# Optimization experiments

Hardware: AMD Instinct MI355X
Metric: run time of the kernel (lower is better)

The kernel has to match this reference:

```python
import jax, jax.numpy as jnp
import numpy as np

N_NODES = 50000
N_EDGES = 800000
UNITS = 128
IN_F = 5


def _sage(x, src, dst, inv_deg, Wl, bl, Wr, n):
    # PyG SAGEConv (mean aggr): out = lin_l(mean_{j in N(i)} x_j) + lin_r(x_i)
    agg = jax.ops.segment_sum(x[src], dst, num_segments=n) * inv_deg  # [n, F]
    return agg @ Wl + bl + x @ Wr


def setup_inputs() -> dict:
    key = jax.random.key(0)
    ks = jax.random.split(key, 16)
    x = jax.random.normal(ks[0], (N_NODES, IN_F), dtype=jnp.float32)
    x = x.at[:, 2].set(0.0)  # do_not_flip flag column: all zeros so no -inf masking
    edge_index = jax.random.randint(ks[1], (2, N_EDGES), 0, N_NODES, dtype=jnp.int64)
    batch = jnp.zeros((N_NODES,), dtype=jnp.int32)

    def lin(k, fi, fo):
        s = 1.0 / np.sqrt(fi)
        return jax.random.uniform(k, (fi, fo), jnp.float32, -s, s)

    inp = {
        "x": x, "edge_index": edge_index, "batch": batch,
        # conv_first: SAGEConv(5, units)
        "Wl1": lin(ks[2], IN_F, UNITS), "bl1": jnp.zeros((UNITS,), jnp.float32), "Wr1": lin(ks[3], IN_F, UNITS),
        # conv_common[0]
        "Wl2": lin(ks[4], UNITS, UNITS), "bl2": jnp.zeros((UNITS,), jnp.float32), "Wr2": lin(ks[5], UNITS, UNITS),
        # conv_actor[0]: SAGEConv(units, 1)
        "Wla": lin(ks[6], UNITS, 1), "bla": jnp.zeros((1,), jnp.float32), "Wra": lin(ks[7], UNITS, 1),
        # conv_critic[0]
        "Wlc": lin(ks[8], UNITS, UNITS), "blc": jnp.zeros((UNITS,), jnp.float32), "Wrc": lin(ks[9], UNITS, UNITS),
        # final_critic Linear(units, 1)
        "Wf": lin(ks[10], UNITS, 1), "bf": jnp.zeros((1,), jnp.float32),
    }
    return inp


def reference(x, edge_index, batch, Wl1, bl1, Wr1, Wl2, bl2, Wr2, Wla, bla, Wra, Wlc, blc, Wrc, Wf, bf):
    n = x.shape[0]
    src, dst = edge_index[0], edge_index[1]
    deg = jax.ops.segment_sum(jnp.ones((src.shape[0],), x.dtype), dst, num_segments=n)
    inv_deg = (1.0 / jnp.maximum(deg, 1.0))[:, None]

    do_not_flip = x[:, 2] != 0.0  # [n]

    h = jnp.tanh(_sage(x, src, dst, inv_deg, Wl1, bl1, Wr1, n))
    h = jnp.tanh(_sage(h, src, dst, inv_deg, Wl2, bl2, Wr2, n))

    x_actor = _sage(h, src, dst, inv_deg, Wla, bla, Wra, n)  # [n, 1]
    x_actor = jnp.where(do_not_flip[:, None], -jnp.inf, x_actor)
    x_actor = jax.nn.log_softmax(x_actor, axis=0)

    x_critic = jax.lax.stop_gradient(h)
    x_critic = _sage(x_critic, src, dst, inv_deg, Wlc, blc, Wrc, n)
    x_critic = x_critic @ Wf + bf  # [n, 1]
    # global_mean_pool over batch (1 graph here)
    num_graphs = 1
    gsum = jax.ops.segment_sum(x_critic, batch, num_segments=num_graphs)
    gcnt = jax.ops.segment_sum(jnp.ones((n,), x.dtype), batch, num_segments=num_graphs)
    x_critic = jnp.tanh(gsum / jnp.maximum(gcnt, 1.0)[:, None])
    return (x_actor, x_critic)
```

## Files before the change

kernel.cpp:

```cpp
#include <hip/hip_runtime.h>
#include <cmath>


#define SCAN_B 256

typedef short short8 __attribute__((ext_vector_type(8)));
typedef float f32x4 __attribute__((ext_vector_type(4)));
typedef float f32x2 __attribute__((ext_vector_type(2)));

__device__ __forceinline__ unsigned short f2b(float f) {
    union { float f; unsigned int u; } v; v.f = f;
    unsigned int r = (v.u + 0x7FFFu + ((v.u >> 16) & 1u)) >> 16;
    return (unsigned short)r;
}
__device__ __forceinline__ float b2f_lo(unsigned int u) {
    union { unsigned int u; float f; } v; v.u = u << 16; return v.f;
}
__device__ __forceinline__ float b2f_hi(unsigned int u) {
    union { unsigned int u; float f; } v; v.u = u & 0xFFFF0000u; return v.f;
}

__global__ void k_count(const int* __restrict__ ei, int* __restrict__ deg, int E) {
    int e = blockIdx.x * 256 + threadIdx.x;
    if (e >= E) return;
    atomicAdd(&deg[ei[E + e]], 1);
}

__global__ void k_blocksum(const int* __restrict__ deg, int* __restrict__ bsum, int n) {
    __shared__ int sd[SCAN_B];
    int i = blockIdx.x * SCAN_B + threadIdx.x;
    sd[threadIdx.x] = (i < n) ? deg[i] : 0;
    __syncthreads();
    for (int s = SCAN_B / 2; s > 0; s >>= 1) {
        if (threadIdx.x < s) sd[threadIdx.x] += sd[threadIdx.x + s];
        __syncthreads();
    }
    if (threadIdx.x == 0) bsum[blockIdx.x] = sd[0];
}

__global__ void k_scan_bsum(int* __restrict__ bsum, int nb) {
    __shared__ int sd[1024];
    int t = threadIdx.x;
    int v = (t < nb) ? bsum[t] : 0;
    sd[t] = v;
    __syncthreads();
    for (int off = 1; off < 1024; off <<= 1) {
        int add = (t >= off) ? sd[t - off] : 0;
        __syncthreads();
        sd[t] += add;
        __syncthreads();
    }
    if (t < nb) bsum[t] = sd[t] - v;
}

__global__ void k_scan_final(const int* __restrict__ deg, const int* __restrict__ bsum,
                             int* __restrict__ row_ptr, int* __restrict__ fill_pos,
                             float* __restrict__ inv_deg, int n) {
    __shared__ int sd[SCAN_B];
    int t = threadIdx.x;
    int i = blockIdx.x * SCAN_B + t;
    int v = (i < n) ? deg[i] : 0;
    sd[t] = v;
    __syncthreads();
    for (int off = 1; off < SCAN_B; off <<= 1) {
        int add = (t >= off) ? sd[t - off] : 0;
        __syncthreads();
        sd[t] += add;
        __syncthreads();
    }
    if (i < n) {
        int excl = bsum[blockIdx.x] + sd[t] - v;
        row_ptr[i] = excl;
        fill_pos[i] = excl;
        inv_deg[i] = 1.0f / fmaxf((float)v, 1.0f);
        if (i == n - 1) row_ptr[n] = excl + v;
    }
}

__global__ void k_fill(const int* __restrict__ ei, int* __restrict__ fill_pos,
                       int* __restrict__ edge_src, int E) {
    int e = blockIdx.x * 256 + threadIdx.x;
    if (e >= E) return;
    int src = ei[e];
    int dst = ei[E + e];
    int pos = atomicAdd(&fill_pos[dst], 1);
    edge_src[pos] = src;
}

__global__ void k_agg0(const float* __restrict__ x, const int* __restrict__ row_ptr,
                       const int* __restrict__ edge_src, const float* __restrict__ inv_deg,
                       float* __restrict__ agg0, int n) {
    int i = blockIdx.x * 256 + threadIdx.x;
    if (i >= n) return;
    float a0 = 0, a1 = 0, a2 = 0, a3 = 0, a4 = 0;
    int s = row_ptr[i], e = row_ptr[i + 1];
    for (int t = s; t < e; ++t) {
        const float* xp = x + (size_t)edge_src[t] * 5;
        a0 += xp[0]; a1 += xp[1]; a2 += xp[2]; a3 += xp[3]; a4 += xp[4];
    }
    float iv = inv_deg[i];
    float* o = agg0 + (size_t)i * 5;
    o[0] = a0 * iv; o[1] = a1 * iv; o[2] = a2 * iv; o[3] = a3 * iv; o[4] = a4 * iv;
}

__global__ void k_h1(const float* __restrict__ x, const float* __restrict__ agg0,
                     const float* __restrict__ Wl1, const float* __restrict__ bl1,
                     const float* __restrict__ Wr1, unsigned short* __restrict__ Acat,
                     unsigned int* __restrict__ H1f8u, int n) {
    __shared__ float sA[8][5], sX[8][5];
    int ty = threadIdx.y, tx = threadIdx.x;
    int node = blockIdx.x * 8 + ty;
    if (node < n && tx < 5) {
        sA[ty][tx] = agg0[(size_t)node * 5 + tx];
        sX[ty][tx] = x[(size_t)node * 5 + tx];
    }
    __syncthreads();
    if (node >= n) return;
    int j0 = tx * 4;
    float4 acc = *(const float4*)(bl1 + j0);
#pragma unroll
    for (int k = 0; k < 5; k++) {
        float4 wl = *(const float4*)(Wl1 + k * 128 + j0);
        float4 wr = *(const float4*)(Wr1 + k * 128 + j0);
        float a = sA[ty][k], xx = sX[ty][k];
        acc.x += a * wl.x + xx * wr.x;
        acc.y += a * wl.y + xx * wr.y;
        acc.z += a * wl.z + xx * wr.z;
        acc.w += a * wl.w + xx * wr.w;
    }
    float t0 = tanhf(acc.x), t1 = tanhf(acc.y), t2 = tanhf(acc.z), t3 = tanhf(acc.w);
    uint2 bw;
    bw.x = (unsigned int)f2b(t0) | ((unsigned int)f2b(t1) << 16);
    bw.y = (unsigned int)f2b(t2) | ((unsigned int)f2b(t3) << 16);
    *(uint2*)(Acat + (size_t)node * 256 + 128 + j0) = bw;
    int p = __builtin_amdgcn_cvt_pk_fp8_f32(t0, t1, 0, false);
    p = __builtin_amdgcn_cvt_pk_fp8_f32(t2, t3, p, true);
    H1f8u[(size_t)node * 32 + tx] = (unsigned int)p;
}

__global__ void k_aggc(const unsigned int* __restrict__ H1f8u, const int* __restrict__ row_ptr,
                       const int* __restrict__ edge_src, const float* __restrict__ inv_deg,
                       unsigned short* __restrict__ Acat, int n, int c) {
    int tid = threadIdx.x;
    int grp = tid >> 4;
    int r = tid & 15;
    int node = blockIdx.x * 16 + grp;
    if (node >= n) return;
    int s = row_ptr[node], e = row_ptr[node + 1];
    const unsigned int* base = H1f8u + c * 16 + r;
    float s0 = 0.f, s1 = 0.f, s2 = 0.f, s3 = 0.f;
    int t = s;
    for (; t + 1 < e; t += 2) {
        unsigned int u0 = base[(size_t)edge_src[t] * 32];
        unsigned int u1 = base[(size_t)edge_src[t + 1] * 32];
        f32x2 lo = __builtin_amdgcn_cvt_pk_f32_fp8(u0, false);
        f32x2 hi = __builtin_amdgcn_cvt_pk_f32_fp8(u0, true);
        s0 += lo[0]; s1 += lo[1]; s2 += hi[0]; s3 += hi[1];
        lo = __builtin_amdgcn_cvt_pk_f32_fp8(u1, false);
        hi = __builtin_amdgcn_cvt_pk_f32_fp8(u1, true);
        s0 += lo[0]; s1 += lo[1]; s2 += hi[0]; s3 += hi[1];
    }
    if (t < e) {
        unsigned int u0 = base[(size_t)edge_src[t] * 32];
        f32x2 lo = __builtin_amdgcn_cvt_pk_f32_fp8(u0, false);
        f32x2 hi = __builtin_amdgcn_cvt_pk_f32_fp8(u0, true);
        s0 += lo[0]; s1 += lo[1]; s2 += hi[0]; s3 += hi[1];
    }
    float iv = inv_deg[node];
    uint2 w;
    w.x = (unsigned int)f2b(s0 * iv) | ((unsigned int)f2b(s1 * iv) << 16);
    w.y = (unsigned int)f2b(s2 * iv) | ((unsigned int)f2b(s3 * iv) << 16);
    *(uint2*)(Acat + (size_t)node * 256 + c * 64 + r * 4) = w;
}

__global__ void k_prepw(const float* __restrict__ Wl2, const float* __restrict__ Wr2,
                        unsigned short* __restrict__ WT) {
    int j = blockIdx.x;
    int k = threadIdx.x;
    float v = (k < 128) ? Wl2[(size_t)k * 128 + j] : Wr2[(size_t)(k - 128) * 128 + j];
    WT[(size_t)j * 256 + k] = f2b(v);
}

__global__ void k_prep(const float* __restrict__ Wlc, const float* __restrict__ blc,
                       const float* __restrict__ Wrc, const float* __restrict__ Wf,
                       const float* __restrict__ bf, float* __restrict__ wcomb) {
    int k = threadIdx.x;
    float sl = 0.f, sr = 0.f;
    for (int j = 0; j < 128; j++) {
        float wf = Wf[j];
        sl += Wlc[(size_t)k * 128 + j] * wf;
        sr += Wrc[(size_t)k * 128 + j] * wf;
    }
    wcomb[k] = sl;
    wcomb[128 + k] = sr;
    __shared__ float sd[128];
    sd[k] = blc[k] * Wf[k];
    __syncthreads();
    for (int s = 64; s > 0; s >>= 1) {
        if (k < s) sd[k] += sd[k + s];
        __syncthreads();
    }
    if (k == 0) wcomb[256] = sd[0] + bf[0];
}

__global__ void k_h2_mfma_dots(const unsigned short* __restrict__ Acat,
                               const unsigned short* __restrict__ WT,
                               const float* __restrict__ bl2,
                               const float* __restrict__ Wla,
                               const float* __restrict__ Wra,
                               const float* __restrict__ wcomb,
                               float2* __restrict__ pp, float2* __restrict__ self, int n) {
    int wave = threadIdx.x >> 6;
    int lane = threadIdx.x & 63;
    int r = lane & 15;
    int g = lane >> 4;
    int rowbase = blockIdx.x * 64 + wave * 16;
    int arow = rowbase + r;
    if (arow > n - 1) arow = n - 1;

    short8 a[8];
    const short* ap = (const short*)(Acat + (size_t)arow * 256 + g * 8);
#pragma unroll
    for (int kk = 0; kk < 8; kk++)
        a[kk] = *(const short8*)(ap + kk * 32);

    float ppa[4] = {0, 0, 0, 0}, ppc[4] = {0, 0, 0, 0};
    float pra[4] = {0, 0, 0, 0}, prc[4] = {0, 0, 0, 0};

#pragma unroll
    for (int nt = 0; nt < 8; nt++) {
        f32x4 acc = {0.f, 0.f, 0.f, 0.f};
        const short* bp = (const short*)(WT + (size_t)(nt * 16 + r) * 256 + g * 8);
#pragma unroll
        for (int kk = 0; kk < 8; kk++) {
            short8 b = *(const short8*)(bp + kk * 32);
            acc = __builtin_amdgcn_mfma_f32_16x16x32_bf16(a[kk], b, acc, 0, 0, 0);
        }
        int col = nt * 16 + r;
        float bj  = bl2[col];
        float wa  = Wla[col];
        float wra = Wra[col];
        float wcl = wcomb[col];
        float wcr = wcomb[128 + col];
#pragma unroll
        for (int q = 0; q < 4; q++) {
            float t = tanhf(acc[q] + bj);
            ppa[q] += t * wa;
            ppc[q] += t * wcl;
            pra[q] += t * wra;
            prc[q] += t * wcr;
        }
    }
#pragma unroll
    for (int q = 0; q < 4; q++) {
#pragma unroll
        for (int off = 8; off >= 1; off >>= 1) {
            ppa[q] += __shfl_xor(ppa[q], off);
            ppc[q] += __shfl_xor(ppc[q], off);
            pra[q] += __shfl_xor(pra[q], off);
            prc[q] += __shfl_xor(prc[q], off);
        }
    }
    if (r == 0) {
#pragma unroll
        for (int q = 0; q < 4; q++) {
            int rr = rowbase + g * 4 + q;
            if (rr < n) {
                pp[rr]   = make_float2(ppa[q], ppc[q]);
                self[rr] = make_float2(pra[q], prc[q]);
            }
        }
    }
}

__global__ void k_sagg(const float2* __restrict__ pp, const float2* __restrict__ self,
                       const int* __restrict__ row_ptr, const int* __restrict__ edge_src,
                       const float* __restrict__ inv_deg, const float* __restrict__ x,
                       const float* __restrict__ bla, const float* __restrict__ wcomb,
                       float* __restrict__ actor_s, float* __restrict__ critic_v, int n) {
    int i = blockIdx.x * 256 + threadIdx.x;
    if (i >= n) return;
    int s = row_ptr[i], e = row_ptr[i + 1];
    float sa = 0.f, sc = 0.f;
    for (int t = s; t < e; ++t) {
        float2 v = pp[edge_src[t]];
        sa += v.x; sc += v.y;
    }
    float iv = inv_deg[i];
    float2 sf = self[i];
    float a = sa * iv + sf.x + bla[0];
    if (x[(size_t)i * 5 + 2] != 0.0f) a = -INFINITY;
    actor_s[i] = a;
    critic_v[i] = sc * iv + sf.y + wcomb[256];
}

__global__ void k_reduce(const float* __restrict__ actor_s, const float* __restrict__ critic_v,
                         float* __restrict__ scalars, float* __restrict__ d_out, int n) {
    __shared__ float sm[1024], ss[1024], sc[1024];
    int t = threadIdx.x;
    float m = -INFINITY, sum = 0.f, cs = 0.f;
    for (int i = t; i < n; i += 1024) {
        cs += critic_v[i];
        float s = actor_s[i];
        if (s == -INFINITY) continue;
        if (s > m) {
            sum = sum * expf(m - s);
            m = s;
        }
        sum += expf(s - m);
    }
    sm[t] = m; ss[t] = sum; sc[t] = cs;
    __syncthreads();
    for (int s2 = 512; s2 > 0; s2 >>= 1) {
        if (t < s2) {
            float m2 = sm[t + s2], v2 = ss[t + s2];
            float M = fmaxf(sm[t], m2);
            if (M == -INFINITY) {
                ss[t] = 0.f;
            } else {
                ss[t] = ss[t] * expf(sm[t] - M) + v2 * expf(m2 - M);
            }
            sm[t] = M;
            sc[t] += sc[t + s2];
        }
        __syncthreads();
    }
    if (t == 0) {
        scalars[0] = sm[0] + logf(ss[0]);
        d_out[n] = tanhf(sc[0] / (float)n);
    }
}

__global__ void k_final(const float* __restrict__ actor_s, const float* __restrict__ scalars,
                        float* __restrict__ d_out, int n) {
    int i = blockIdx.x * 256 + threadIdx.x;
    if (i >= n) return;
    d_out[i] = actor_s[i] - scalars[0];
}

extern "C" void kernel_launch(void* const* d_in, const int* in_sizes, int n_in,
                              void* d_out, int out_size, void* d_ws, size_t ws_size,
                              hipStream_t stream) {
    const float* x   = (const float*)d_in[0];
    const int*   ei  = (const int*)d_in[1];
    const float* Wl1 = (const float*)d_in[3];
    const float* bl1 = (const float*)d_in[4];
    const float* Wr1 = (const float*)d_in[5];
    const float* Wl2 = (const float*)d_in[6];
    const float* bl2 = (const float*)d_in[7];
    const float* Wr2 = (const float*)d_in[8];
    const float* Wla = (const float*)d_in[9];
    const float* bla = (const float*)d_in[10];
    const float* Wra = (const float*)d_in[11];
    const float* Wlc = (const float*)d_in[12];
    const float* blc = (const float*)d_in[13];
    const float* Wrc = (const float*)d_in[14];
    const float* Wf  = (const float*)d_in[15];
    const float* bf  = (const float*)d_in[16];

    const int n = in_sizes[0] / 5;
    const int E = in_sizes[1] / 2;
    float* out = (float*)d_out;

    char* w = (char*)d_ws;
    auto alloc = [&](size_t bytes) -> void* {
        void* p = (void*)w;
        w += (bytes + 255) & ~(size_t)255;
        return p;
    };
    int* deg      = (int*)alloc((size_t)n * 4);
    int* row_ptr  = (int*)alloc((size_t)(n + 1) * 4);
    int* fill_pos = (int*)alloc((size_t)n * 4);
    int* bsum     = (int*)alloc(1024 * 4);
    int* edge_src = (int*)alloc((size_t)E * 4);
    float* inv_deg = (float*)alloc((size_t)n * 4);
    float* agg0    = (float*)alloc((size_t)n * 5 * 4);
    unsigned short* Acat = (unsigned short*)alloc((size_t)n * 256 * 2);
    unsigned int* H1f8u  = (unsigned int*)alloc((size_t)n * 128);
    unsigned short* WT   = (unsigned short*)alloc((size_t)128 * 256 * 2);
    float2* pp     = (float2*)alloc((size_t)n * 8);
    float2* selfb  = (float2*)alloc((size_t)n * 8);
    float* actor_s = (float*)alloc((size_t)n * 4);
    float* critic_v= (float*)alloc((size_t)n * 4);
    float* wcomb   = (float*)alloc(260 * 4);
    float* scalars = (float*)alloc(16);

    hipMemsetAsync(deg, 0, (size_t)n * 4, stream);

    const int nbE = (E + 255) / 256;
    const int nbN = (n + 255) / 256;
    const int nbScan = (n + SCAN_B - 1) / SCAN_B;

    k_count<<<nbE, 256, 0, stream>>>(ei, deg, E);
    k_blocksum<<<nbScan, SCAN_B, 0, stream>>>(deg, bsum, n);
    k_scan_bsum<<<1, 1024, 0, stream>>>(bsum, nbScan);
    k_scan_final<<<nbScan, SCAN_B, 0, stream>>>(deg, bsum, row_ptr, fill_pos, inv_deg, n);
    k_fill<<<nbE, 256, 0, stream>>>(ei, fill_pos, edge_src, E);

    k_agg0<<<nbN, 256, 0, stream>>>(x, row_ptr, edge_src, inv_deg, agg0, n);
    k_h1<<<(n + 7) / 8, dim3(32, 8), 0, stream>>>(x, agg0, Wl1, bl1, Wr1, Acat, H1f8u, n);

    k_aggc<<<(n + 15) / 16, 256, 0, stream>>>(H1f8u, row_ptr, edge_src, inv_deg, Acat, n, 0);
    k_aggc<<<(n + 15) / 16, 256, 0, stream>>>(H1f8u, row_ptr, edge_src, inv_deg, Acat, n, 1);

    k_prepw<<<128, 256, 0, stream>>>(Wl2, Wr2, WT);
    k_prep<<<1, 128, 0, stream>>>(Wlc, blc, Wrc, Wf, bf, wcomb);
    k_h2_mfma_dots<<<(n + 63) / 64, 256, 0, stream>>>(Acat, WT, bl2, Wla, Wra, wcomb,
                                                      pp, selfb, n);

    k_sagg<<<nbN, 256, 0, stream>>>(pp, selfb, row_ptr, edge_src, inv_deg, x,
                                    bla, wcomb, actor_s, critic_v, n);
    k_reduce<<<1, 1024, 0, stream>>>(actor_s, critic_v, scalars, out, n);
    k_final<<<nbN, 256, 0, stream>>>(actor_s, scalars, out, n);
}
```

Baseline: 254.7 us.

## Build CSR via two-level bucketed binning instead of global atomic counting sort

Replaces the global-atomic degree count, three-kernel scan and atomic scatter fill with a two-level bucket sort. Edges are first binned into 128-node buckets using shared-memory histograms and per-block atomic reservations, then each bucket is sorted locally in LDS to produce row_ptr, inv_deg and edge_src. This reduces global atomic contention and the scattered writes, and drops the memset. In exchange it makes an extra pass over the edges through an intermediate packed array. The packing assumes source indices fit in 25 bits and at most 512 buckets.

Result: faster. 212.7 us (-16.5%).

```diff
diff --git a/kernel.cpp b/kernel.cpp
--- a/kernel.cpp
+++ b/kernel.cpp
@@ -2,7 +2,11 @@
 #include <cmath>
 
 
-#define SCAN_B 256
+#define NPB_SHIFT 7
+#define NPB 128
+#define MAXNB 512
+#define HBLK 192
+#define CHUNK 8192
 
 typedef short short8 __attribute__((ext_vector_type(8)));
 typedef float f32x4 __attribute__((ext_vector_type(4)));
@@ -13,79 +17,113 @@
     unsigned int r = (v.u + 0x7FFFu + ((v.u >> 16) & 1u)) >> 16;
     return (unsigned short)r;
 }
-__device__ __forceinline__ float b2f_lo(unsigned int u) {
-    union { unsigned int u; float f; } v; v.u = u << 16; return v.f;
-}
-__device__ __forceinline__ float b2f_hi(unsigned int u) {
-    union { unsigned int u; float f; } v; v.u = u & 0xFFFF0000u; return v.f;
-}
-
-__global__ void k_count(const int* __restrict__ ei, int* __restrict__ deg, int E) {
-    int e = blockIdx.x * 256 + threadIdx.x;
-    if (e >= E) return;
-    atomicAdd(&deg[ei[E + e]], 1);
-}
-
-__global__ void k_blocksum(const int* __restrict__ deg, int* __restrict__ bsum, int n) {
-    __shared__ int sd[SCAN_B];
-    int i = blockIdx.x * SCAN_B + threadIdx.x;
-    sd[threadIdx.x] = (i < n) ? deg[i] : 0;
-    __syncthreads();
-    for (int s = SCAN_B / 2; s > 0; s >>= 1) {
-        if (threadIdx.x < s) sd[threadIdx.x] += sd[threadIdx.x + s];
-        __syncthreads();
-    }
-    if (threadIdx.x == 0) bsum[blockIdx.x] = sd[0];
-}
-
-__global__ void k_scan_bsum(int* __restrict__ bsum, int nb) {
-    __shared__ int sd[1024];
+
+
+__global__ void kb_hist(const int* __restrict__ ei, int* __restrict__ partial, int E, int NB) {
+    __shared__ int h[MAXNB];
+    for (int i = threadIdx.x; i < NB; i += 256) h[i] = 0;
+    __syncthreads();
+    for (int i = blockIdx.x * 256 + threadIdx.x; i < E; i += 256 * gridDim.x)
+        atomicAdd(&h[ei[E + i] >> NPB_SHIFT], 1);
+    __syncthreads();
+    for (int b = threadIdx.x; b < NB; b += 256)
+        partial[(size_t)b * HBLK + blockIdx.x] = h[b];
+}
+
+__global__ void kb_scan(const int* __restrict__ partial, int* __restrict__ bucket_base,
+                        int* __restrict__ bucket_cur, int NB) {
+    __shared__ int sd[MAXNB];
     int t = threadIdx.x;
-    int v = (t < nb) ? bsum[t] : 0;
-    sd[t] = v;
-    __syncthreads();
-    for (int off = 1; off < 1024; off <<= 1) {
+    int c = 0;
+    if (t < NB) {
+        const int* p = partial + (size_t)t * HBLK;
+        for (int k = 0; k < HBLK; k++) c += p[k];
+    }
+    sd[t] = c;
+    __syncthreads();
+    for (int off = 1; off < MAXNB; off <<= 1) {
         int add = (t >= off) ? sd[t - off] : 0;
         __syncthreads();
         sd[t] += add;
         __syncthreads();
     }
-    if (t < nb) bsum[t] = sd[t] - v;
-}
-
-__global__ void k_scan_final(const int* __restrict__ deg, const int* __restrict__ bsum,
-                             int* __restrict__ row_ptr, int* __restrict__ fill_pos,
-                             float* __restrict__ inv_deg, int n) {
-    __shared__ int sd[SCAN_B];
+    if (t < NB) {
+        int excl = sd[t] - c;
+        bucket_base[t] = excl;
+        bucket_cur[t] = excl;
+        if (t == NB - 1) bucket_base[NB] = sd[t];
+    }
+}
+
+__global__ void kb_bin(const int* __restrict__ ei, int* __restrict__ bucket_cur,
+                       unsigned int* __restrict__ binned, int E, int NB) {
+    __shared__ int lcnt[MAXNB];
+    __shared__ int lbase[MAXNB];
+    __shared__ int lcur[MAXNB];
+    int s = blockIdx.x * CHUNK;
+    int e = min(E, s + CHUNK);
+    for (int i = threadIdx.x; i < NB; i += 256) lcnt[i] = 0;
+    __syncthreads();
+    for (int i = s + threadIdx.x; i < e; i += 256)
+        atomicAdd(&lcnt[ei[E + i] >> NPB_SHIFT], 1);
+    __syncthreads();
+    for (int b = threadIdx.x; b < NB; b += 256) {
+        int c = lcnt[b];
+        lbase[b] = c ? atomicAdd(&bucket_cur[b], c) : 0;
+        lcur[b] = 0;
+    }
+    __syncthreads();
+    for (int i = s + threadIdx.x; i < e; i += 256) {
+        int src = ei[i];
+        int dst = ei[E + i];
+        int b = dst >> NPB_SHIFT;
+        int pos = lbase[b] + atomicAdd(&lcur[b], 1);
+        binned[pos] = (unsigned int)src | ((unsigned int)(dst & (NPB - 1)) << 25);
+    }
+}
+
+__global__ void kb_csr(const unsigned int* __restrict__ binned, const int* __restrict__ bucket_base,
+                       int* __restrict__ row_ptr, float* __restrict__ inv_deg,
+                       int* __restrict__ edge_src, int n, int NB) {
+    __shared__ int lcnt[NPB];
+    __shared__ int lexcl[NPB];
+    __shared__ int lcur[NPB];
+    int b = blockIdx.x;
     int t = threadIdx.x;
-    int i = blockIdx.x * SCAN_B + t;
-    int v = (i < n) ? deg[i] : 0;
-    sd[t] = v;
-    __syncthreads();
-    for (int off = 1; off < SCAN_B; off <<= 1) {
-        int add = (t >= off) ? sd[t - off] : 0;
-        __syncthreads();
-        sd[t] += add;
-        __syncthreads();
-    }
-    if (i < n) {
-        int excl = bsum[blockIdx.x] + sd[t] - v;
-        row_ptr[i] = excl;
-        fill_pos[i] = excl;
-        inv_deg[i] = 1.0f / fmaxf((float)v, 1.0f);
-        if (i == n - 1) row_ptr[n] = excl + v;
-    }
-}
-
-__global__ void k_fill(const int* __restrict__ ei, int* __restrict__ fill_pos,
-                       int* __restrict__ edge_src, int E) {
-    int e = blockIdx.x * 256 + threadIdx.x;
-    if (e >= E) return;
-    int src = ei[e];
-    int dst = ei[E + e];
-    int pos = atomicAdd(&fill_pos[dst], 1);
-    edge_src[pos] = src;
-}
+    int base = bucket_base[b], end = bucket_base[b + 1];
+    lcnt[t] = 0;
+    lcur[t] = 0;
+    __syncthreads();
+    for (int i = base + t; i < end; i += NPB)
+        atomicAdd(&lcnt[binned[i] >> 25], 1);
+    __syncthreads();
+    int v = lcnt[t];
+    lexcl[t] = v;
+    __syncthreads();
+    for (int off = 1; off < NPB; off <<= 1) {
+        int add = (t >= off) ? lexcl[t - off] : 0;
+        __syncthreads();
+        lexcl[t] += add;
+        __syncthreads();
+    }
+    int excl = lexcl[t] - v;
+    __syncthreads();
+    lexcl[t] = excl;
+    __syncthreads();
+    int node = b * NPB + t;
+    if (node < n) {
+        row_ptr[node] = base + excl;
+        inv_deg[node] = 1.0f / fmaxf((float)v, 1.0f);
+    }
+    if (b == 0 && t == 0) row_ptr[n] = bucket_base[NB];
+    for (int i = base + t; i < end; i += NPB) {
+        unsigned int u = binned[i];
+        int l = u >> 25;
+        int pos = lexcl[l] + atomicAdd(&lcur[l], 1);
+        edge_src[base + pos] = (int)(u & 0x01FFFFFFu);
+    }
+}
+
 
 __global__ void k_agg0(const float* __restrict__ x, const int* __restrict__ row_ptr,
                        const int* __restrict__ edge_src, const float* __restrict__ inv_deg,
@@ -360,6 +398,7 @@
 
     const int n = in_sizes[0] / 5;
     const int E = in_sizes[1] / 2;
+    const int NB = (n + NPB - 1) >> NPB_SHIFT;
     float* out = (float*)d_out;
 
     char* w = (char*)d_ws;
@@ -368,10 +407,11 @@
         w += (bytes + 255) & ~(size_t)255;
         return p;
     };
-    int* deg      = (int*)alloc((size_t)n * 4);
+    int* partial     = (int*)alloc((size_t)MAXNB * HBLK * 4);
+    int* bucket_base = (int*)alloc((size_t)(MAXNB + 1) * 4);
+    int* bucket_cur  = (int*)alloc((size_t)MAXNB * 4);
+    unsigned int* binned = (unsigned int*)alloc((size_t)E * 4);
     int* row_ptr  = (int*)alloc((size_t)(n + 1) * 4);
-    int* fill_pos = (int*)alloc((size_t)n * 4);
-    int* bsum     = (int*)alloc(1024 * 4);
     int* edge_src = (int*)alloc((size_t)E * 4);
     float* inv_deg = (float*)alloc((size_t)n * 4);
     float* agg0    = (float*)alloc((size_t)n * 5 * 4);
@@ -385,17 +425,12 @@
     float* wcomb   = (float*)alloc(260 * 4);
     float* scalars = (float*)alloc(16);
 
-    hipMemsetAsync(deg, 0, (size_t)n * 4, stream);
-
-    const int nbE = (E + 255) / 256;
     const int nbN = (n + 255) / 256;
-    const int nbScan = (n + SCAN_B - 1) / SCAN_B;
-
-    k_count<<<nbE, 256, 0, stream>>>(ei, deg, E);
-    k_blocksum<<<nbScan, SCAN_B, 0, stream>>>(deg, bsum, n);
-    k_scan_bsum<<<1, 1024, 0, stream>>>(bsum, nbScan);
-    k_scan_final<<<nbScan, SCAN_B, 0, stream>>>(deg, bsum, row_ptr, fill_pos, inv_deg, n);
-    k_fill<<<nbE, 256, 0, stream>>>(ei, fill_pos, edge_src, E);
+
+    kb_hist<<<HBLK, 256, 0, stream>>>(ei, partial, E, NB);
+    kb_scan<<<1, MAXNB, 0, stream>>>(partial, bucket_base, bucket_cur, NB);
+    kb_bin<<<(E + CHUNK - 1) / CHUNK, 256, 0, stream>>>(ei, bucket_cur, binned, E, NB);
+    kb_csr<<<NB, NPB, 0, stream>>>(binned, bucket_base, row_ptr, inv_deg, edge_src, n, NB);
 
     k_agg0<<<nbN, 256, 0, stream>>>(x, row_ptr, edge_src, inv_deg, agg0, n);
     k_h1<<<(n + 7) / 8, dim3(32, 8), 0, stream>>>(x, agg0, Wl1, bl1, Wr1, Acat, H1f8u, n);
```
